# Optimization experiments

Hardware: AMD Instinct MI355X
Metric: run time of the kernel (lower is better)

Reference implementation:

```python
import jax, jax.numpy as jnp
import numpy as np
from jax.scipy.special import erfinv

N_CHUNKS = 64
D = 128          # input_dim
O = 256          # output_dim
B = 4096         # batch (batch_last)
P = D // 2       # number of 2D pairs

def get_borders_cdf_grid(n):
    # CDF (Gaussian-quantile) spaced grid borders; clip probs to keep endpoints finite
    p = jnp.clip(jnp.arange(n + 1, dtype=jnp.float32) / n, 0.5 / n, 1.0 - 0.5 / n)
    return jnp.sqrt(2.0) * erfinv(2.0 * p - 1.0)

BORDERS = get_borders_cdf_grid(N_CHUNKS)  # (n_chunks+1,)


def setup_inputs() -> dict:
    key = jax.random.key(0)
    ks = jax.random.split(key, 5)
    s = 1.0 / np.sqrt(D)
    return {
        "x": jax.random.normal(ks[0], (D, B), dtype=jnp.float32),
        "weight_lmKAN": jnp.ones((1,), dtype=jnp.float32),
        "apply_relu_linear": 1,
        "func_parameter": jax.random.uniform(ks[1], (N_CHUNKS + 1, N_CHUNKS + 1, O, P), minval=-s, maxval=s, dtype=jnp.float32),
        "scale_parameters": jnp.ones((D,), dtype=jnp.float32),
        "bias_parameters": jnp.zeros((D,), dtype=jnp.float32),
        "W_linear": jax.random.uniform(ks[2], (O, D), minval=-s, maxval=s, dtype=jnp.float32),
        "bias_linear": jax.random.uniform(ks[3], (O,), minval=-s, maxval=s, dtype=jnp.float32),
    }


def lmkan_2d(fp, x):
    """2D bucketized grid lookup + bilinear interpolation.
    fp: (G, G, O, P) with G = n_chunks+1; x: (D, B) -> out (O, B)."""
    n = fp.shape[0] - 1
    pairs = x.reshape(P, 2, -1)                      # adjacent-channel pairs
    eps = 1e-6
    x1 = jnp.clip(pairs[:, 0], BORDERS[0], BORDERS[-1] - eps)  # (P, B)
    x2 = jnp.clip(pairs[:, 1], BORDERS[0], BORDERS[-1] - eps)
    i = jnp.clip(jnp.searchsorted(BORDERS, x1, side='right') - 1, 0, n - 1)
    j = jnp.clip(jnp.searchsorted(BORDERS, x2, side='right') - 1, 0, n - 1)
    t1 = (x1 - BORDERS[i]) / (BORDERS[i + 1] - BORDERS[i])      # (P, B) in [0,1)
    t2 = (x2 - BORDERS[j]) / (BORDERS[j + 1] - BORDERS[j])
    pidx = jnp.arange(P)[:, None]                    # (P, 1) -> broadcasts to (P, B)

    def corner(ii, jj, w):
        g = fp[ii, jj, :, pidx]                      # gather -> (P, B, O)
        return jnp.einsum('pb,pbo->ob', w, g)

    return (corner(i,     j,     (1.0 - t1) * (1.0 - t2))
          + corner(i + 1, j,     t1 * (1.0 - t2))
          + corner(i,     j + 1, (1.0 - t1) * t2)
          + corner(i + 1, j + 1, t1 * t2))


def reference(x, weight_lmKAN, apply_relu_linear, func_parameter, scale_parameters, bias_parameters, W_linear, bias_linear):
    # relu_last=True branch of the original forward
    linear_out = W_linear @ x + bias_linear[:, None]         # (O, B)
    if apply_relu_linear:
        linear_out = jax.nn.relu(linear_out)
    xs = x * scale_parameters[:, None] + bias_parameters[:, None]  # apply_scale / apply_bias
    # apply_tanh=False
    lmkan_out = lmkan_2d(func_parameter, xs)                 # (O, B)
    return 1.0 * linear_out + weight_lmKAN * lmkan_out
```

## Files before the change

### kernel.cpp

```cpp
#include <hip/hip_runtime.h>
#include <hip/hip_fp16.h>


#define NB 4096
#define ND 128
#define NO 256
#define NP 64
#define NG 65
#define PANEL 16384
#define FPT_ELEMS ((size_t)NG * NG * PANEL)
#define FPT_BYTES (FPT_ELEMS * 2)
#define PART_FLOATS ((size_t)8 * NB * NO)
#define NBLK 512
#define BARS 64
#define CTRL_U32 4096

typedef float f32x4 __attribute__((ext_vector_type(4)));
union Pack8 { __half h[8]; uint4 v; };

__device__ __forceinline__ int bsearch65(const float* B, float v) {
  int lo = 0, hi = 65;
  while (lo < hi) {
    int m = (lo + hi) >> 1;
    if (B[m] <= v) lo = m + 1; else hi = m;
  }
  int i = lo - 1;
  return i < 0 ? 0 : (i > 63 ? 63 : i);
}

__device__ __forceinline__ void borders_init(float* borders, int t) {
  if (t < 65) {
    float pk = fminf(fmaxf((float)t * (1.0f / 64.0f), 0.0078125f), 0.9921875f);
    borders[t] = 1.41421356237309515f * erfinvf(2.0f * pk - 1.0f);
  }
}

__device__ __forceinline__ void xcd_barrier(unsigned* ctrl, int xcd, int ph) {
  __syncthreads();
  if (threadIdx.x == 0) {
    unsigned* c = ctrl + (xcd * 8 + ph) * 64;
    __hip_atomic_fetch_add(c, 1u, __ATOMIC_RELAXED, __HIP_MEMORY_SCOPE_AGENT);
    for (int it = 0; it < 24; ++it) {
      if (__hip_atomic_load(c, __ATOMIC_RELAXED,
                            __HIP_MEMORY_SCOPE_AGENT) >= BARS) break;
      __builtin_amdgcn_s_sleep(64);
    }
  }
  __syncthreads();
}

__global__ __launch_bounds__(256) void lmkan_transpose3(
    const float* __restrict__ src, __half* __restrict__ dst,
    unsigned* __restrict__ ctrl) {
  const int panel = blockIdx.x;
  const int t = threadIdx.x;
  __shared__ __half lds[256 * 72];

  if (panel == 0) {
#pragma unroll
    for (int k = 0; k < 16; ++k) ctrl[t + 256 * k] = 0u;
  }

  const f32x4* s4 = reinterpret_cast<const f32x4*>(src + (size_t)panel * PANEL);
#pragma unroll
  for (int k = 0; k < 16; ++k) {
    int idx4 = t + 256 * k;
    f32x4 v = __builtin_nontemporal_load(&s4[idx4]);
    int o = idx4 >> 4;
    int p0 = (idx4 & 15) * 4;
    int p0s = p0 ^ (((o >> 3) & 15) << 2);
    union { __half2 h2[2]; uint2 u; } pk;
    pk.h2[0] = __floats2half2_rn(v[0], v[1]);
    pk.h2[1] = __floats2half2_rn(v[2], v[3]);
    *reinterpret_cast<uint2*>(&lds[o * 72 + p0s]) = pk.u;
  }
  __syncthreads();

  const int l = t & 63, w = t >> 6;
  const int o0 = (l & 31) * 8;
  const int swz = (l & 15) << 2;
#pragma unroll
  for (int ss = 0; ss < 8; ++ss) {
    int p = ss * 8 + w * 2 + (l >> 5);
    int prow = ((p & ~3) ^ swz) + (p & 3);
    Pack8 pk;
#pragma unroll
    for (int r = 0; r < 8; ++r) pk.h[r] = lds[(o0 + r) * 72 + prow];
    *reinterpret_cast<uint4*>(dst + ((size_t)panel * 64 + p) * NO + o0) = pk.v;
  }
}

__device__ __forceinline__ void fma4h(float acc[4], float w, uint2 v) {
  __half2 h0 = *reinterpret_cast<__half2*>(&v.x);
  __half2 h1 = *reinterpret_cast<__half2*>(&v.y);
  float2 f0 = __half22float2(h0);
  float2 f1 = __half22float2(h1);
  acc[0] = fmaf(w, f0.x, acc[0]);
  acc[1] = fmaf(w, f0.y, acc[1]);
  acc[2] = fmaf(w, f1.x, acc[2]);
  acc[3] = fmaf(w, f1.y, acc[3]);
}

__global__ __launch_bounds__(256, 2) void lmkan_gather9(
    const float* __restrict__ x, const float* __restrict__ scale,
    const float* __restrict__ biasp, const __half* __restrict__ fpt,
    float* __restrict__ part, unsigned* __restrict__ ctrl) {
  const int xcd = blockIdx.x & 7;
  const int m   = blockIdx.x >> 3;
  const int t = threadIdx.x;
  const int w = t >> 6;
  const int l = t & 63;
  const int loff = 4 * l;

  __shared__ float borders[66];
  __shared__ int jb[64];
  __shared__ float4 w4[64];

  borders_init(borders, t);
  __syncthreads();

  float acc[16][4] = {};

  for (int ph = 0; ph < 8; ++ph) {
    const int p = 8 * xcd + ph;
    if (t < 64) {
      const int b = m * 64 + t;
      float x1 = x[(size_t)(2 * p) * NB + b]     * scale[2 * p]     + biasp[2 * p];
      float x2 = x[(size_t)(2 * p + 1) * NB + b] * scale[2 * p + 1] + biasp[2 * p + 1];
      const float lo = borders[0];
      const float hi = borders[64] - 1e-6f;
      x1 = fminf(fmaxf(x1, lo), hi);
      x2 = fminf(fmaxf(x2, lo), hi);
      int i = bsearch65(borders, x1);
      int j = bsearch65(borders, x2);
      float t1 = (x1 - borders[i]) / (borders[i + 1] - borders[i]);
      float t2 = (x2 - borders[j]) / (borders[j + 1] - borders[j]);
      jb[t] = ((i * NG + j) * 64 + p) * NO;
      w4[t] = make_float4((1.0f - t1) * (1.0f - t2),
                          (1.0f - t1) * t2,
                          t1 * (1.0f - t2),
                          t1 * t2);
    }
    __syncthreads();
#pragma unroll
    for (int bb = 0; bb < 16; ++bb) {
      const int bl = w * 16 + bb;
      const float4 wv = w4[bl];
      const __half* q = fpt + jb[bl] + loff;
      uint2 vA = *reinterpret_cast<const uint2*>(q);
      uint2 vB = *reinterpret_cast<const uint2*>(q + PANEL);
      uint2 vC = *reinterpret_cast<const uint2*>(q + 65 * PANEL);
      uint2 vD = *reinterpret_cast<const uint2*>(q + 66 * PANEL);
      fma4h(acc[bb], wv.x, vA);
      fma4h(acc[bb], wv.y, vB);
      fma4h(acc[bb], wv.z, vC);
      fma4h(acc[bb], wv.w, vD);
    }
    if (ph < 7) xcd_barrier(ctrl, xcd, ph);
  }

#pragma unroll
  for (int bb = 0; bb < 16; ++bb) {
    const int b = m * 64 + w * 16 + bb;
    *reinterpret_cast<float4*>(&part[((size_t)xcd * NB + b) * NO + loff]) =
        make_float4(acc[bb][0], acc[bb][1], acc[bb][2], acc[bb][3]);
  }
}

__global__ __launch_bounds__(256) void lmkan_linear2(
    const float* __restrict__ x, const float* __restrict__ W,
    const float* __restrict__ bias_l, const int* __restrict__ relu_p,
    const float* __restrict__ wlm_p, const float* __restrict__ part,
    float* __restrict__ out) {
  const int b0 = blockIdx.x * 32;
  const int t = threadIdx.x;
  __shared__ __align__(16) float xs[32 * 132];

#pragma unroll
  for (int k = 0; k < 16; ++k) {
    int idx = t + 256 * k;
    int d = idx >> 5, bb = idx & 31;
    xs[bb * 132 + d] = x[(size_t)d * NB + b0 + bb];
  }
  __syncthreads();

  float acc[32];
#pragma unroll
  for (int bb = 0; bb < 32; ++bb) acc[bb] = 0.0f;

  const float4* W4 = reinterpret_cast<const float4*>(W + (size_t)t * ND);
#pragma unroll 8
  for (int d4 = 0; d4 < 32; ++d4) {
    float4 wv = W4[d4];
#pragma unroll
    for (int bb = 0; bb < 32; ++bb) {
      float4 xv = *reinterpret_cast<const float4*>(&xs[bb * 132 + d4 * 4]);
      acc[bb] = fmaf(wv.x, xv.x, acc[bb]);
      acc[bb] = fmaf(wv.y, xv.y, acc[bb]);
      acc[bb] = fmaf(wv.z, xv.z, acc[bb]);
      acc[bb] = fmaf(wv.w, xv.w, acc[bb]);
    }
  }

  const float bias = bias_l[t];
  const int rl = relu_p[0];
  const float wlm = wlm_p[0];
  float* orow = out + (size_t)t * NB + b0;
#pragma unroll 4
  for (int bb = 0; bb < 32; ++bb) {
    float lmsum = 0.0f;
    const float* pr = part + (size_t)(b0 + bb) * NO + t;
#pragma unroll
    for (int k = 0; k < 8; ++k) lmsum += pr[(size_t)k * NB * NO];
    float v = acc[bb] + bias;
    if (rl) v = fmaxf(v, 0.0f);
    orow[bb] = v + wlm * lmsum;
  }
}

__global__ __launch_bounds__(64) void lmkan_gather_direct(
    const float* __restrict__ x, const float* __restrict__ scale,
    const float* __restrict__ biasp, const float* __restrict__ W,
    const float* __restrict__ bias_l, const float* __restrict__ wlm_p,
    const int* __restrict__ relu_p, const float* __restrict__ fp,
    float* __restrict__ out) {
  const int b = blockIdx.x;
  const int t = threadIdx.x;

  __shared__ float borders[66];
  __shared__ __align__(16) float xcol[ND];
  __shared__ int pbase[NP];
  __shared__ float4 pw[NP];

  for (int k = t; k < 65; k += 64) {
    float pk = fminf(fmaxf((float)k * (1.0f / 64.0f), 0.0078125f), 0.9921875f);
    borders[k] = 1.41421356237309515f * erfinvf(2.0f * pk - 1.0f);
  }
  xcol[t]      = x[(size_t)t * NB + b];
  xcol[t + 64] = x[(size_t)(t + 64) * NB + b];
  __syncthreads();

  {
    const int p = t;
    float x1 = xcol[2 * p]     * scale[2 * p]     + biasp[2 * p];
    float x2 = xcol[2 * p + 1] * scale[2 * p + 1] + biasp[2 * p + 1];
    const float lo = borders[0];
    const float hi = borders[64] - 1e-6f;
    x1 = fminf(fmaxf(x1, lo), hi);
    x2 = fminf(fmaxf(x2, lo), hi);
    int i = bsearch65(borders, x1);
    int j = bsearch65(borders, x2);
    float t1 = (x1 - borders[i]) / (borders[i + 1] - borders[i]);
    float t2 = (x2 - borders[j]) / (borders[j + 1] - borders[j]);
    pbase[p] = i * NG + j;
    pw[p] = make_float4((1.0f - t1) * (1.0f - t2), t1 * (1.0f - t2),
                        (1.0f - t1) * t2, t1 * t2);
  }
  __syncthreads();

  float acc[4] = {0, 0, 0, 0};
  for (int p = 0; p < NP; ++p) {
    int base = pbase[p];
    float4 wv = pw[p];
#pragma unroll
    for (int k = 0; k < 4; ++k) {
      size_t r = ((size_t)base * NO + (4 * t + k)) * NP + p;
      acc[k] += wv.x * fp[r] + wv.y * fp[r + 65 * PANEL] +
                wv.z * fp[r + PANEL] + wv.w * fp[r + 66 * PANEL];
    }
  }

  const float wlm = wlm_p[0];
  const int rl = relu_p[0];
  const float4* xc4 = reinterpret_cast<const float4*>(xcol);
#pragma unroll
  for (int k = 0; k < 4; ++k) {
    const int o = 4 * t + k;
    const float4* wr = reinterpret_cast<const float4*>(W + (size_t)o * ND);
    float s = 0.0f;
#pragma unroll 8
    for (int d4 = 0; d4 < ND / 4; ++d4) {
      float4 wv = wr[d4];
      float4 xv = xc4[d4];
      s = fmaf(wv.x, xv.x, s);
      s = fmaf(wv.y, xv.y, s);
      s = fmaf(wv.z, xv.z, s);
      s = fmaf(wv.w, xv.w, s);
    }
    s += bias_l[o];
    if (rl) s = fmaxf(s, 0.0f);
    out[(size_t)o * NB + b] = s + wlm * acc[k];
  }
}

extern "C" void kernel_launch(void* const* d_in, const int* in_sizes, int n_in,
                              void* d_out, int out_size, void* d_ws, size_t ws_size,
                              hipStream_t stream) {
  const float* x     = reinterpret_cast<const float*>(d_in[0]);
  const float* wlm   = reinterpret_cast<const float*>(d_in[1]);
  const int*   relu  = reinterpret_cast<const int*>(d_in[2]);
  const float* fp    = reinterpret_cast<const float*>(d_in[3]);
  const float* scale = reinterpret_cast<const float*>(d_in[4]);
  const float* biasp = reinterpret_cast<const float*>(d_in[5]);
  const float* W     = reinterpret_cast<const float*>(d_in[6]);
  const float* bl    = reinterpret_cast<const float*>(d_in[7]);
  float* out = reinterpret_cast<float*>(d_out);

  const size_t need = FPT_BYTES + PART_FLOATS * sizeof(float)
                      + CTRL_U32 * sizeof(unsigned);
  if (ws_size >= need) {
    char* base = reinterpret_cast<char*>(d_ws);
    __half* fpt = reinterpret_cast<__half*>(base);
    float* part = reinterpret_cast<float*>(base + FPT_BYTES);
    unsigned* ctrl = reinterpret_cast<unsigned*>(
        base + FPT_BYTES + PART_FLOATS * sizeof(float));
    lmkan_transpose3<<<NG * NG, 256, 0, stream>>>(fp, fpt, ctrl);
    lmkan_gather9<<<NBLK, 256, 0, stream>>>(x, scale, biasp, fpt, part, ctrl);
    lmkan_linear2<<<NB / 32, 256, 0, stream>>>(x, W, bl, relu, wlm, part, out);
  } else {
    lmkan_gather_direct<<<NB, 64, 0, stream>>>(x, scale, biasp, W, bl, wlm, relu, fp, out);
  }
}
```

Before: 206.7 us.

## Store fp16 table pair-major and bind gather blocks to actual XCC with slab prefetch

The fp16 transposed table is re-laid out so that each pair's full 65x65x256 grid is one contiguous slab, which makes the four bilinear corners nearby in memory. The gather kernel reads the hardware XCC ID and atomically claims a (group, chunk) slot, so each group of 64 blocks really shares one XCD's L2. Each block also prefetches its share of the next pair's slab into L2 before the soft phase barrier, so the later random gathers hit cache. This adds atomics for claiming slots, extra prefetch reads, and a shorter barrier spin. Correctness relies on every slot being claimed, which holds because there are exactly 512 blocks and 512 slots.

```diff
diff --git a/kernel.cpp b/kernel.cpp
--- a/kernel.cpp
+++ b/kernel.cpp
@@ -7,13 +7,16 @@
 #define NO 256
 #define NP 64
 #define NG 65
+#define NPANEL 4225
 #define PANEL 16384
-#define FPT_ELEMS ((size_t)NG * NG * PANEL)
+#define SLAB_ELEMS ((size_t)NPANEL * NO)
+#define SLAB_VEC4 135200
+#define FPT_ELEMS ((size_t)NP * NPANEL * NO)
 #define FPT_BYTES (FPT_ELEMS * 2)
 #define PART_FLOATS ((size_t)8 * NB * NO)
 #define NBLK 512
 #define BARS 64
-#define CTRL_U32 4096
+#define CTRL_U32 8192
 
 typedef float f32x4 __attribute__((ext_vector_type(4)));
 union Pack8 { __half h[8]; uint4 v; };
@@ -35,21 +38,20 @@
   }
 }
 
-__device__ __forceinline__ void xcd_barrier(unsigned* ctrl, int xcd, int ph) {
+__device__ __forceinline__ void phase_wait(unsigned* cline) {
   __syncthreads();
   if (threadIdx.x == 0) {
-    unsigned* c = ctrl + (xcd * 8 + ph) * 64;
-    __hip_atomic_fetch_add(c, 1u, __ATOMIC_RELAXED, __HIP_MEMORY_SCOPE_AGENT);
-    for (int it = 0; it < 24; ++it) {
-      if (__hip_atomic_load(c, __ATOMIC_RELAXED,
+    __hip_atomic_fetch_add(cline, 1u, __ATOMIC_RELAXED, __HIP_MEMORY_SCOPE_AGENT);
+    for (int it = 0; it < 12; ++it) {
+      if (__hip_atomic_load(cline, __ATOMIC_RELAXED,
                             __HIP_MEMORY_SCOPE_AGENT) >= BARS) break;
-      __builtin_amdgcn_s_sleep(64);
-    }
-  }
-  __syncthreads();
-}
-
-__global__ __launch_bounds__(256) void lmkan_transpose3(
+      __builtin_amdgcn_s_sleep(32);
+    }
+  }
+  __syncthreads();
+}
+
+__global__ __launch_bounds__(256) void lmkan_transpose4(
     const float* __restrict__ src, __half* __restrict__ dst,
     unsigned* __restrict__ ctrl) {
   const int panel = blockIdx.x;
@@ -58,7 +60,7 @@
 
   if (panel == 0) {
 #pragma unroll
-    for (int k = 0; k < 16; ++k) ctrl[t + 256 * k] = 0u;
+    for (int k = 0; k < 32; ++k) ctrl[t + 256 * k] = 0u;
   }
 
   const f32x4* s4 = reinterpret_cast<const f32x4*>(src + (size_t)panel * PANEL);
@@ -86,7 +88,7 @@
     Pack8 pk;
 #pragma unroll
     for (int r = 0; r < 8; ++r) pk.h[r] = lds[(o0 + r) * 72 + prow];
-    *reinterpret_cast<uint4*>(dst + ((size_t)panel * 64 + p) * NO + o0) = pk.v;
+    *reinterpret_cast<uint4*>(dst + ((size_t)p * NPANEL + panel) * NO + o0) = pk.v;
   }
 }
 
@@ -101,30 +103,64 @@
   acc[3] = fmaf(w, f1.y, acc[3]);
 }
 
-__global__ __launch_bounds__(256, 2) void lmkan_gather9(
+__device__ __forceinline__ void slab_prefetch(const __half* slabp, int c, int t) {
+  const f32x4* pf = reinterpret_cast<const f32x4*>(slabp);
+  const int tid = c * 256 + t;
+  float s = 0.0f;
+#pragma unroll
+  for (int k = 0; k < 9; ++k) {
+    int i = tid + 16384 * k;
+    if (i < SLAB_VEC4) {
+      f32x4 v = pf[i];
+      s += v[0] + v[3];
+    }
+  }
+  asm volatile("" :: "v"(s));
+}
+
+__global__ __launch_bounds__(256, 2) void lmkan_gather10(
     const float* __restrict__ x, const float* __restrict__ scale,
     const float* __restrict__ biasp, const __half* __restrict__ fpt,
     float* __restrict__ part, unsigned* __restrict__ ctrl) {
-  const int xcd = blockIdx.x & 7;
-  const int m   = blockIdx.x >> 3;
   const int t = threadIdx.x;
   const int w = t >> 6;
   const int l = t & 63;
   const int loff = 4 * l;
 
+  unsigned xcc;
+  asm volatile("s_getreg_b32 %0, hwreg(HW_REG_XCC_ID)" : "=s"(xcc));
+  xcc &= 7;
+
   __shared__ float borders[66];
+  __shared__ int sgc[2];
   __shared__ int jb[64];
   __shared__ float4 w4[64];
 
   borders_init(borders, t);
-  __syncthreads();
-
+  if (t == 0) {
+    int g = -1, c = -1;
+    for (int q = 0; q < 8 && g < 0; ++q) {
+      int gg = ((int)xcc + q) & 7;
+      unsigned cc = __hip_atomic_fetch_add(&ctrl[gg * 64], 1u,
+                        __ATOMIC_RELAXED, __HIP_MEMORY_SCOPE_AGENT);
+      if (cc < (unsigned)BARS) { g = gg; c = (int)cc; }
+    }
+    sgc[0] = g; sgc[1] = c;
+  }
+  __syncthreads();
+  const int g = sgc[0], c = sgc[1];
+  if (g < 0) return;
+
+  unsigned* phcnt = ctrl + 512 + g * 8 * 64;
   float acc[16][4] = {};
 
+  slab_prefetch(fpt + (size_t)(8 * g) * SLAB_ELEMS, c, t);
+
   for (int ph = 0; ph < 8; ++ph) {
-    const int p = 8 * xcd + ph;
+    const int p = 8 * g + ph;
+    const __half* slab = fpt + (size_t)p * SLAB_ELEMS;
     if (t < 64) {
-      const int b = m * 64 + t;
+      const int b = c * 64 + t;
       float x1 = x[(size_t)(2 * p) * NB + b]     * scale[2 * p]     + biasp[2 * p];
       float x2 = x[(size_t)(2 * p + 1) * NB + b] * scale[2 * p + 1] + biasp[2 * p + 1];
       const float lo = borders[0];
@@ -135,7 +171,7 @@
       int j = bsearch65(borders, x2);
       float t1 = (x1 - borders[i]) / (borders[i + 1] - borders[i]);
       float t2 = (x2 - borders[j]) / (borders[j + 1] - borders[j]);
-      jb[t] = ((i * NG + j) * 64 + p) * NO;
+      jb[t] = (i * NG + j) * NO;
       w4[t] = make_float4((1.0f - t1) * (1.0f - t2),
                           (1.0f - t1) * t2,
                           t1 * (1.0f - t2),
@@ -146,23 +182,26 @@
     for (int bb = 0; bb < 16; ++bb) {
       const int bl = w * 16 + bb;
       const float4 wv = w4[bl];
-      const __half* q = fpt + jb[bl] + loff;
+      const __half* q = slab + jb[bl] + loff;
       uint2 vA = *reinterpret_cast<const uint2*>(q);
-      uint2 vB = *reinterpret_cast<const uint2*>(q + PANEL);
-      uint2 vC = *reinterpret_cast<const uint2*>(q + 65 * PANEL);
-      uint2 vD = *reinterpret_cast<const uint2*>(q + 66 * PANEL);
+      uint2 vB = *reinterpret_cast<const uint2*>(q + NO);
+      uint2 vC = *reinterpret_cast<const uint2*>(q + NG * NO);
+      uint2 vD = *reinterpret_cast<const uint2*>(q + NG * NO + NO);
       fma4h(acc[bb], wv.x, vA);
       fma4h(acc[bb], wv.y, vB);
       fma4h(acc[bb], wv.z, vC);
       fma4h(acc[bb], wv.w, vD);
     }
-    if (ph < 7) xcd_barrier(ctrl, xcd, ph);
+    if (ph < 7) {
+      slab_prefetch(slab + SLAB_ELEMS, c, t);
+      phase_wait(phcnt + ph * 64);
+    }
   }
 
 #pragma unroll
   for (int bb = 0; bb < 16; ++bb) {
-    const int b = m * 64 + w * 16 + bb;
-    *reinterpret_cast<float4*>(&part[((size_t)xcd * NB + b) * NO + loff]) =
+    const int b = c * 64 + w * 16 + bb;
+    *reinterpret_cast<float4*>(&part[((size_t)g * NB + b) * NO + loff]) =
         make_float4(acc[bb][0], acc[bb][1], acc[bb][2], acc[bb][3]);
   }
 }
@@ -314,8 +353,8 @@
     float* part = reinterpret_cast<float*>(base + FPT_BYTES);
     unsigned* ctrl = reinterpret_cast<unsigned*>(
         base + FPT_BYTES + PART_FLOATS * sizeof(float));
-    lmkan_transpose3<<<NG * NG, 256, 0, stream>>>(fp, fpt, ctrl);
-    lmkan_gather9<<<NBLK, 256, 0, stream>>>(x, scale, biasp, fpt, part, ctrl);
+    lmkan_transpose4<<<NPANEL, 256, 0, stream>>>(fp, fpt, ctrl);
+    lmkan_gather10<<<NBLK, 256, 0, stream>>>(x, scale, biasp, fpt, part, ctrl);
     lmkan_linear2<<<NB / 32, 256, 0, stream>>>(x, W, bl, relu, wlm, part, out);
   } else {
     lmkan_gather_direct<<<NB, 64, 0, stream>>>(x, scale, biasp, W, bl, wlm, relu, fp, out);
```

Result: slower. 240.9 us (+16.6%).
